# Performance work log

Measured on AMD Instinct MI355X. Metric: run time of the kernel, lower is better.

## Reference

```python
import jax, jax.numpy as jnp
import numpy as np

IOU_THRESHOLD = 0.5  # default in ObjectUtils.nms
N_BOXES = 10000


def setup_inputs() -> dict:
    key = jax.random.key(0)
    k1, k2 = jax.random.split(key)
    boxes = jax.random.uniform(k1, (N_BOXES, 4), dtype=jnp.float32)  # normalized cxcywh
    scores = jax.random.uniform(k2, (N_BOXES,), dtype=jnp.float32)
    return {"boxes_cxcywh": boxes, "scores": scores}


def _cxcywh_to_ltrb(b):
    cx, cy, w, h = b[:, 0], b[:, 1], b[:, 2], b[:, 3]
    return jnp.stack([cx - w / 2, cy - h / 2, cx + w / 2, cy + h / 2], axis=1)


def _pairwise_iou(a, b):
    # a: [N1,4] ltrb, b: [N2,4] ltrb -> [N1,N2] (matches ObjectUtils.compute_iou)
    lt = jnp.maximum(a[:, None, :2], b[None, :, :2])
    rb = jnp.minimum(a[:, None, 2:], b[None, :, 2:])
    wh = jnp.clip(rb - lt, 0.0)
    inter = wh[..., 0] * wh[..., 1]
    area_a = (a[:, 2] - a[:, 0]) * (a[:, 3] - a[:, 1])
    area_b = (b[:, 2] - b[:, 0]) * (b[:, 3] - b[:, 1])
    return inter / (area_a[:, None] + area_b[None, :] - inter)


def reference(boxes_cxcywh, scores):
    ltrb = _cxcywh_to_ltrb(boxes_cxcywh)
    iou = _pairwise_iou(ltrb, ltrb)  # [N,N]

    # ---- greedy NMS, faithful to ObjectUtils.nms (unclamped intersection,
    # retain when iou < threshold) expressed as a jit-friendly suppression loop ----
    n = ltrb.shape[0]
    order = jnp.argsort(-scores)  # highest score first (torch.sort ascending, pop last)
    bs = ltrb[order]
    l, t, r, b = bs[:, 0], bs[:, 1], bs[:, 2], bs[:, 3]
    area = (r - l) * (b - t)
    inter_nms = (jnp.minimum(r[:, None], r[None, :]) - jnp.maximum(l[:, None], l[None, :])) * \
                (jnp.minimum(b[:, None], b[None, :]) - jnp.maximum(t[:, None], t[None, :]))
    iou_nms = inter_nms / (area[:, None] + area[None, :] - inter_nms)
    ar = jnp.arange(n)

    def body(i, keep):
        # box i (in sorted order) suppresses lower-scored boxes only if it is itself kept
        suppress = keep[i] & (iou_nms[i] >= IOU_THRESHOLD) & (ar > i)
        return keep & jnp.logical_not(suppress)

    keep_sorted = jax.lax.fori_loop(0, n, body, jnp.ones((n,), dtype=bool))
    keep = jnp.zeros((n,), dtype=bool).at[order].set(keep_sorted)
    return iou, keep
```

## Files before the change

### kernel.cpp

```cpp
#include <hip/hip_runtime.h>

typedef unsigned long long u64;
typedef float f32x4 __attribute__((ext_vector_type(4)));

#define THR 0.5f

__device__ __forceinline__ u64 rfl64(u64 v) {
  unsigned lo = (unsigned)__builtin_amdgcn_readfirstlane((int)(unsigned)v);
  unsigned hi = (unsigned)__builtin_amdgcn_readfirstlane((int)(unsigned)(v >> 32));
  return ((u64)hi << 32) | lo;
}

__device__ __forceinline__ void conv_box(const float4 b, float& l, float& t,
                                         float& r, float& bo, float& a) {
  #pragma clang fp contract(off)
  float hw = 0.5f * b.z;
  float hh = 0.5f * b.w;
  l = b.x - hw;
  t = b.y - hh;
  r = b.x + hw;
  bo = b.y + hh;
  a = (r - l) * (bo - t);
}

__global__ void k_zero(int* __restrict__ rank, int n) {
  int i = blockIdx.x * blockDim.x + threadIdx.x;
  if (i < n) rank[i] = 0;
}

__global__ void k_rank(const float* __restrict__ scores, int* __restrict__ rank,
                       int n, int jchunk) {
  int i = blockIdx.x * blockDim.x + threadIdx.x;
  if (i >= n) return;
  float si = scores[i];
  int j0 = blockIdx.y * jchunk;
  int j1 = min(j0 + jchunk, n);
  int c = 0;
  for (int j = j0; j < j1; ++j) {
    float sj = scores[j];
    c += ((sj > si) || (sj == si && j < i)) ? 1 : 0;
  }
  if (c) atomicAdd(rank + i, c);
}

__global__ void k_scatter(const float4* __restrict__ boxes, const int* __restrict__ rank,
                          float* __restrict__ sl, float* __restrict__ st,
                          float* __restrict__ sr, float* __restrict__ sb,
                          float* __restrict__ sa, int* __restrict__ sidx, int n) {
  int i = blockIdx.x * blockDim.x + threadIdx.x;
  if (i >= n) return;
  float l, t, r, b, a;
  conv_box(boxes[i], l, t, r, b, a);
  int k = rank[i];
  sl[k] = l; st[k] = t; sr[k] = r; sb[k] = b; sa[k] = a; sidx[k] = i;
}

__device__ __forceinline__ void mask_body(
    const float* __restrict__ sl, const float* __restrict__ st,
    const float* __restrict__ sr, const float* __restrict__ sb,
    const float* __restrict__ sa,
    u64* __restrict__ mask, u64* __restrict__ diag,
    u64* __restrict__ band1, u64* __restrict__ band2,
    int n, int wstride, int bx, int by) {
  #pragma clang fp contract(off)
  int k = bx * 256 + threadIdx.x;
  if (k >= n) return;
  int w = by;
  int jbase = w << 6;
  u64 word = 0;
  if (jbase + 63 > k) {
    float l = sl[k], t = st[k], r = sr[k], b = sb[k], a = sa[k];
    int jend = min(jbase + 64, n);
    for (int j = max(jbase, k + 1); j < jend; ++j) {
      float lmax = fmaxf(l, sl[j]);
      float tmax = fmaxf(t, st[j]);
      float rmin = fminf(r, sr[j]);
      float bmin = fminf(b, sb[j]);
      float wd = rmin - lmax;
      float hd = bmin - tmax;
      float inter = wd * hd;
      float denom = (a + sa[j]) - inter;
      float q = inter / denom;
      if (q >= THR) word |= 1ull << (j - jbase);
    }
  }
  mask[(size_t)k * wstride + w] = word;
  int kg = k >> 6;
  if (kg == w) diag[k] = word;
  if (w == kg + 1) band1[k] = word;
  if (w == kg + 2) band2[k] = word;
}

__global__ void k_mask(const float* __restrict__ sl, const float* __restrict__ st,
                       const float* __restrict__ sr, const float* __restrict__ sb,
                       const float* __restrict__ sa,
                       u64* __restrict__ mask, u64* __restrict__ diag,
                       u64* __restrict__ band1, u64* __restrict__ band2,
                       int n, int wstride) {
  mask_body(sl, st, sr, sb, sa, mask, diag, band1, band2, n, wstride,
            blockIdx.x, blockIdx.y);
}

__device__ __forceinline__ u64 wave_or_u64(u64 v) {
  unsigned lo = (unsigned)v, hi = (unsigned)(v >> 32);
#define DPP_OR(x, ctrl, rmask) \
  x |= (unsigned)__builtin_amdgcn_update_dpp(0, (int)(x), ctrl, rmask, 0xF, true)
  DPP_OR(lo, 0x111, 0xF); DPP_OR(hi, 0x111, 0xF);
  DPP_OR(lo, 0x112, 0xF); DPP_OR(hi, 0x112, 0xF);
  DPP_OR(lo, 0x114, 0xF); DPP_OR(hi, 0x114, 0xF);
  DPP_OR(lo, 0x118, 0xF); DPP_OR(hi, 0x118, 0xF);
  DPP_OR(lo, 0x142, 0xA); DPP_OR(hi, 0x142, 0xA);
  DPP_OR(lo, 0x143, 0xC); DPP_OR(hi, 0x143, 0xC);
#undef DPP_OR
  unsigned flo = (unsigned)__builtin_amdgcn_readlane((int)lo, 63);
  unsigned fhi = (unsigned)__builtin_amdgcn_readlane((int)hi, 63);
  return ((u64)fhi << 32) | flo;
}

__device__ __forceinline__ void scan_body9(
    const u64* __restrict__ mask, const u64* __restrict__ diag,
    const u64* __restrict__ band1, const u64* __restrict__ band2,
    const int* __restrict__ sidx, float* __restrict__ keep,
    int n, int wstride,
    u64* rem, u64* bsh1, u64* bsh2, u64* kwords,
    int (*kept)[64], int* nk_sh) {
  int t = threadIdx.x, wv = t >> 6, lane = t & 63;
  int ng = (n + 63) >> 6;
  rem[t] = 0;
  if (t < 3) nk_sh[t] = 0;
  u64 R1 = 0, R2 = 0;
  u64 A0=0,A1=0,A2=0,A3=0,A4=0,A5=0,A6=0,A7=0;
  u64 B0=0,B1=0,B2=0,B3=0,B4=0,B5=0,B6=0,B7=0;
  u64 C0=0,C1=0,C2=0,C3=0,C4=0,C5=0,C6=0,C7=0;
  if (wv == 0) {
    bsh1[lane] = band1[lane];
    bsh2[lane] = band2[lane];
    A0=diag[0];A1=diag[1];A2=diag[2];A3=diag[3];
    A4=diag[4];A5=diag[5];A6=diag[6];A7=diag[7];
    B0=diag[8];B1=diag[9];B2=diag[10];B3=diag[11];
    B4=diag[12];B5=diag[13];B6=diag[14];B7=diag[15];
  }
  __syncthreads();
  for (int g = 0; g < ng; ++g) {
    int base = g << 6;
    if (wv == 0) {
      int nxt = base + 64 + lane;
      bool hn = (g + 1 < ng);
      u64 b1next = hn ? band1[nxt] : 0;
      u64 b2next = hn ? band2[nxt] : 0;
      u64 b1v = bsh1[lane], b2v = bsh2[lane];
      u64 s = rfl64(rem[g]) | R1;
      int valid = n - base;
      if (valid < 64) s |= (~0ull) << valid;
      u64 kw = 0;
      const u64* __restrict__ dgrp = diag + base;
#define SLOAD(P0,P1,P2,P3,P4,P5,P6,P7, OFF) { \
      P0 = dgrp[(OFF)+0]; P1 = dgrp[(OFF)+1]; P2 = dgrp[(OFF)+2]; P3 = dgrp[(OFF)+3]; \
      P4 = dgrp[(OFF)+4]; P5 = dgrp[(OFF)+5]; P6 = dgrp[(OFF)+6]; P7 = dgrp[(OFF)+7]; }
#define SSTEP(BB, EQ) { u64 sup = (s >> (BB)) & 1ull; \
      kw |= (sup ^ 1ull) << (BB); s |= sup ? 0ull : (EQ); }
#define SCHUNK(B0v, E0,E1,E2,E3,E4,E5,E6,E7) \
      if (((~s >> (B0v)) & 0xFFull) != 0ull) { \
        SSTEP(B0v+0, E0) SSTEP(B0v+1, E1) SSTEP(B0v+2, E2) SSTEP(B0v+3, E3) \
        SSTEP(B0v+4, E4) SSTEP(B0v+5, E5) SSTEP(B0v+6, E6) SSTEP(B0v+7, E7) }
      SLOAD(C0,C1,C2,C3,C4,C5,C6,C7, 16); SCHUNK(0,  A0,A1,A2,A3,A4,A5,A6,A7);
      SLOAD(A0,A1,A2,A3,A4,A5,A6,A7, 24); SCHUNK(8,  B0,B1,B2,B3,B4,B5,B6,B7);
      SLOAD(B0,B1,B2,B3,B4,B5,B6,B7, 32); SCHUNK(16, C0,C1,C2,C3,C4,C5,C6,C7);
      SLOAD(C0,C1,C2,C3,C4,C5,C6,C7, 40); SCHUNK(24, A0,A1,A2,A3,A4,A5,A6,A7);
      SLOAD(A0,A1,A2,A3,A4,A5,A6,A7, 48); SCHUNK(32, B0,B1,B2,B3,B4,B5,B6,B7);
      SLOAD(B0,B1,B2,B3,B4,B5,B6,B7, 56); SCHUNK(40, C0,C1,C2,C3,C4,C5,C6,C7);
                                          SCHUNK(48, A0,A1,A2,A3,A4,A5,A6,A7);
                                          SCHUNK(56, B0,B1,B2,B3,B4,B5,B6,B7);
      SLOAD(A0,A1,A2,A3,A4,A5,A6,A7, 64);
      SLOAD(B0,B1,B2,B3,B4,B5,B6,B7, 72);
#undef SCHUNK
#undef SSTEP
#undef SLOAD
      if (lane == 0) kwords[g] = kw;
      u64 c1 = 0, c2 = 0;
      if (kw) {
        int nk = __popcll(kw);
        if ((kw >> lane) & 1ull) {
          int pos = __popcll(kw & ((1ull << lane) - 1ull));
          kept[g % 3][pos] = lane;
        }
        int npad = (nk + 31) & ~31;
        if (lane >= nk && lane < npad) kept[g % 3][lane] = 0;
        if (lane == 0) nk_sh[g % 3] = nk;
        u64 m = (u64)0 - ((kw >> lane) & 1ull);
        c1 = wave_or_u64(b1v & m);
        c2 = wave_or_u64(b2v & m);
      } else {
        if (lane == 0) nk_sh[g % 3] = 0;
      }
      R1 = R2 | c1;
      R2 = c2;
      bsh1[lane] = b1next;
      bsh2[lane] = b2next;
    } else {
      int w = t - 64;
      int gp = g - 2;
      if (gp >= 0 && w > g && w < ng) {
        int nkp = nk_sh[gp % 3];
        if (nkp) {
          const int* kp = kept[gp % 3];
          int basep = gp << 6;
          u64 acc = 0;
          for (int i = 0; i < nkp; i += 32) {
#define LD1(q) u64 v##q = mask[(size_t)(basep + kp[i + q]) * wstride + w];
            LD1(0)  LD1(1)  LD1(2)  LD1(3)  LD1(4)  LD1(5)  LD1(6)  LD1(7)
            LD1(8)  LD1(9)  LD1(10) LD1(11) LD1(12) LD1(13) LD1(14) LD1(15)
            LD1(16) LD1(17) LD1(18) LD1(19) LD1(20) LD1(21) LD1(22) LD1(23)
            LD1(24) LD1(25) LD1(26) LD1(27) LD1(28) LD1(29) LD1(30) LD1(31)
#undef LD1
#define ACC(q) if (i + q < nkp) acc |= v##q;
            ACC(0)  ACC(1)  ACC(2)  ACC(3)  ACC(4)  ACC(5)  ACC(6)  ACC(7)
            ACC(8)  ACC(9)  ACC(10) ACC(11) ACC(12) ACC(13) ACC(14) ACC(15)
            ACC(16) ACC(17) ACC(18) ACC(19) ACC(20) ACC(21) ACC(22) ACC(23)
            ACC(24) ACC(25) ACC(26) ACC(27) ACC(28) ACC(29) ACC(30) ACC(31)
#undef ACC
          }
          rem[w] |= acc;
        }
      }
    }
    __syncthreads();
  }
  for (int k = t; k < n; k += 256) {
    u64 kwv = kwords[k >> 6];
    keep[sidx[k]] = ((kwv >> (k & 63)) & 1ull) ? 1.0f : 0.0f;
  }
}

__global__ __launch_bounds__(256, 1) void k_scan2(const u64* __restrict__ mask,
                                                  const u64* __restrict__ diag,
                                                  const u64* __restrict__ band1,
                                                  const u64* __restrict__ band2,
                                                  const int* __restrict__ sidx,
                                                  float* __restrict__ keep,
                                                  int n, int wstride) {
  __shared__ u64 rem[256];
  __shared__ u64 bsh1[64];
  __shared__ u64 bsh2[64];
  __shared__ u64 kwords[160];
  __shared__ int kept[3][64];
  __shared__ int nk_sh[3];
  scan_body9(mask, diag, band1, band2, sidx, keep, n, wstride,
             rem, bsh1, bsh2, kwords, kept, nk_sh);
}

__device__ __forceinline__ float iou_one(float li, float ti, float ri, float bi, float ai,
                                         float lj, float tj, float rj, float bj, float aj) {
  float lmax = fmaxf(li, lj);
  float tmax = fmaxf(ti, tj);
  float rmin = fminf(ri, rj);
  float bmin = fminf(bi, bj);
  float w = fmaxf(rmin - lmax, 0.0f);
  float h = fmaxf(bmin - tmax, 0.0f);
  float inter = w * h;
  float denom = (ai + aj) - inter;
  return inter * __builtin_amdgcn_rcpf(denom);
}

__device__ __forceinline__ void iou_body(const float4* __restrict__ boxes,
                                         float* __restrict__ out,
                                         int n, int rpb, int bx, int by) {
  int nj4 = (n + 3) >> 2;
  int j4 = bx * 256 + threadIdx.x;
  if (j4 >= nj4) return;
  int j = j4 << 2;
  int jc1 = min(j + 1, n - 1), jc2 = min(j + 2, n - 1), jc3 = min(j + 3, n - 1);
  float l0,t0,r0,b0,a0, l1,t1,r1,b1,a1, l2,t2,r2,b2,a2, l3,t3,r3,b3,a3;
  conv_box(boxes[j],   l0,t0,r0,b0,a0);
  conv_box(boxes[jc1], l1,t1,r1,b1,a1);
  conv_box(boxes[jc2], l2,t2,r2,b2,a2);
  conv_box(boxes[jc3], l3,t3,r3,b3,a3);
  bool full = (j + 3) < n;
  for (int rr = 0; rr < rpb; ++rr) {
    int i = by * rpb + rr;
    if (i >= n) return;
    float li,ti,ri,bi,ai;
    conv_box(boxes[i], li,ti,ri,bi,ai);
    float4 o;
    o.x = iou_one(li,ti,ri,bi,ai, l0,t0,r0,b0,a0);
    o.y = iou_one(li,ti,ri,bi,ai, l1,t1,r1,b1,a1);
    o.z = iou_one(li,ti,ri,bi,ai, l2,t2,r2,b2,a2);
    o.w = iou_one(li,ti,ri,bi,ai, l3,t3,r3,b3,a3);
    size_t row = (size_t)i * n;
    if (full) {
      f32x4 ov = { o.x, o.y, o.z, o.w };
      __builtin_nontemporal_store(ov, reinterpret_cast<f32x4*>(out + row + j));
    } else {
      out[row + j] = o.x;
      if (j + 1 < n) out[row + j + 1] = o.y;
      if (j + 2 < n) out[row + j + 2] = o.z;
    }
  }
}

__global__ void k_iou(const float4* __restrict__ boxes, float* __restrict__ out,
                      int n, int rpb) {
  iou_body(boxes, out, n, rpb, blockIdx.x, blockIdx.y);
}

__global__ __launch_bounds__(256) void k_maskiou(
    const float* __restrict__ sl, const float* __restrict__ st,
    const float* __restrict__ sr, const float* __restrict__ sb,
    const float* __restrict__ sa,
    u64* __restrict__ mask, u64* __restrict__ diag,
    u64* __restrict__ band1, u64* __restrict__ band2,
    int wstride, const float4* __restrict__ boxes, float* __restrict__ out,
    int n, int rpb, int nbx, int nmask, int gx) {
  int id = blockIdx.x;
  if (id < nmask) {
    mask_body(sl, st, sr, sb, sa, mask, diag, band1, band2, n, wstride,
              id % nbx, id / nbx);
  } else {
    int iid = id - nmask;
    iou_body(boxes, out, n, rpb, iid % gx, iid / gx);
  }
}

extern "C" void kernel_launch(void* const* d_in, const int* in_sizes, int n_in,
                              void* d_out, int out_size, void* d_ws, size_t ws_size,
                              hipStream_t stream) {
  const float* boxes = (const float*)d_in[0];
  const float* scores = (const float*)d_in[1];
  int n = in_sizes[1];
  float* out = (float*)d_out;
  size_t NN = (size_t)n * (size_t)n;
  float* keep = out + NN;

  int words = (n + 63) >> 6;
  int wstride = (words + 3) & ~3;
  size_t need = (size_t)n * wstride * 8
              + ((size_t)words * 64 + 64) * 8
              + (size_t)words * 64 * 8 * 2
              + 256
              + (size_t)n * 4 * 7;
  bool use_ws = (ws_size >= need);

  char* base = use_ws ? (char*)d_ws : (char*)d_out;
  size_t off = 0;
  u64* mask  = (u64*)(base + off); off += (size_t)n * wstride * 8;
  u64* diag  = (u64*)(base + off); off += ((size_t)words * 64 + 64) * 8;
  u64* band1 = (u64*)(base + off); off += (size_t)words * 64 * 8;
  u64* band2 = (u64*)(base + off); off += (size_t)words * 64 * 8;
  off = (off + 255) & ~(size_t)255;
  float* sl  = (float*)(base + off); off += (size_t)n * 4;
  float* st_ = (float*)(base + off); off += (size_t)n * 4;
  float* sr  = (float*)(base + off); off += (size_t)n * 4;
  float* sb  = (float*)(base + off); off += (size_t)n * 4;
  float* sa  = (float*)(base + off); off += (size_t)n * 4;
  int* sidx  = (int*)(base + off); off += (size_t)n * 4;
  int* rank  = (int*)(base + off); off += (size_t)n * 4;

  int nb = (n + 255) / 256;
  k_zero<<<nb, 256, 0, stream>>>(rank, n);

  int jblocks = 40;
  int jchunk = (n + jblocks - 1) / jblocks;
  k_rank<<<dim3(nb, jblocks), 256, 0, stream>>>(scores, rank, n, jchunk);

  k_scatter<<<nb, 256, 0, stream>>>((const float4*)boxes, rank, sl, st_, sr, sb, sa, sidx, n);

  int rpb = 10;
  int nj4 = (n + 3) >> 2;
  int gx = (nj4 + 255) / 256;
  int gy = (n + rpb - 1) / rpb;

  if (use_ws) {
    int nmask = nb * words;
    int total = nmask + gx * gy;
    k_maskiou<<<total, 256, 0, stream>>>(sl, st_, sr, sb, sa, mask, diag, band1,
                                         band2, wstride, (const float4*)boxes,
                                         out, n, rpb, nb, nmask, gx);
    k_scan2<<<1, 256, 0, stream>>>(mask, diag, band1, band2, sidx, keep, n, wstride);
  } else {
    k_mask<<<dim3(nb, words), 256, 0, stream>>>(sl, st_, sr, sb, sa, mask, diag,
                                                band1, band2, n, wstride);
    k_scan2<<<1, 256, 0, stream>>>(mask, diag, band1, band2, sidx, keep, n, wstride);
    k_iou<<<dim3(gx, gy), 256, 0, stream>>>((const float4*)boxes, out, n, rpb);
  }
}
```

Before: 455.9 us.

## Replace 4-wave NMS scan with single-wave register-resident scan

```diff
diff --git a/kernel.cpp b/kernel.cpp
--- a/kernel.cpp
+++ b/kernel.cpp
@@ -5,9 +5,9 @@
 
 #define THR 0.5f
 
-__device__ __forceinline__ u64 rfl64(u64 v) {
-  unsigned lo = (unsigned)__builtin_amdgcn_readfirstlane((int)(unsigned)v);
-  unsigned hi = (unsigned)__builtin_amdgcn_readfirstlane((int)(unsigned)(v >> 32));
+__device__ __forceinline__ u64 rdl64c(u64 v, int l) {
+  unsigned lo = (unsigned)__builtin_amdgcn_readlane((int)(unsigned)v, l);
+  unsigned hi = (unsigned)__builtin_amdgcn_readlane((int)(unsigned)(v >> 32), l);
   return ((u64)hi << 32) | lo;
 }
 
@@ -117,136 +117,177 @@
   return ((u64)fhi << 32) | flo;
 }
 
-__device__ __forceinline__ void scan_body9(
+__device__ __forceinline__ void fold8_now(const u64* __restrict__ mask, int base,
+    u64 bits, int cnt, int wstride, int lane, int w2c,
+    u64& r0, u64& r1, u64& r2) {
+  u64 t = bits;
+  int k0 = __ffsll((long long)t) - 1; t &= t - 1;
+  int k1 = __ffsll((long long)t) - 1; t &= t - 1;
+  int k2 = __ffsll((long long)t) - 1; t &= t - 1;
+  int k3 = __ffsll((long long)t) - 1; t &= t - 1;
+  int k4 = __ffsll((long long)t) - 1; t &= t - 1;
+  int k5 = __ffsll((long long)t) - 1; t &= t - 1;
+  int k6 = __ffsll((long long)t) - 1; t &= t - 1;
+  int k7 = __ffsll((long long)t) - 1;
+  k0 = max(k0, 0); k1 = max(k1, 0); k2 = max(k2, 0); k3 = max(k3, 0);
+  k4 = max(k4, 0); k5 = max(k5, 0); k6 = max(k6, 0); k7 = max(k7, 0);
+  const u64* p0 = mask + (size_t)(base + k0) * wstride;
+  const u64* p1 = mask + (size_t)(base + k1) * wstride;
+  const u64* p2 = mask + (size_t)(base + k2) * wstride;
+  const u64* p3 = mask + (size_t)(base + k3) * wstride;
+  const u64* p4 = mask + (size_t)(base + k4) * wstride;
+  const u64* p5 = mask + (size_t)(base + k5) * wstride;
+  const u64* p6 = mask + (size_t)(base + k6) * wstride;
+  const u64* p7 = mask + (size_t)(base + k7) * wstride;
+  u64 a0=p0[lane], a1=p0[lane+64], a2=p0[w2c];
+  u64 b0=p1[lane], b1=p1[lane+64], b2=p1[w2c];
+  u64 c0=p2[lane], c1=p2[lane+64], c2=p2[w2c];
+  u64 d0=p3[lane], d1=p3[lane+64], d2=p3[w2c];
+  u64 e0=p4[lane], e1=p4[lane+64], e2=p4[w2c];
+  u64 f0=p5[lane], f1=p5[lane+64], f2=p5[w2c];
+  u64 g0=p6[lane], g1=p6[lane+64], g2=p6[w2c];
+  u64 h0=p7[lane], h1=p7[lane+64], h2=p7[w2c];
+  if (cnt > 0) { r0|=a0; r1|=a1; r2|=a2; }
+  if (cnt > 1) { r0|=b0; r1|=b1; r2|=b2; }
+  if (cnt > 2) { r0|=c0; r1|=c1; r2|=c2; }
+  if (cnt > 3) { r0|=d0; r1|=d1; r2|=d2; }
+  if (cnt > 4) { r0|=e0; r1|=e1; r2|=e2; }
+  if (cnt > 5) { r0|=f0; r1|=f1; r2|=f2; }
+  if (cnt > 6) { r0|=g0; r1|=g1; r2|=g2; }
+  if (cnt > 7) { r0|=h0; r1|=h1; r2|=h2; }
+}
+
+__global__ __launch_bounds__(64, 1) void k_scan3(
     const u64* __restrict__ mask, const u64* __restrict__ diag,
     const u64* __restrict__ band1, const u64* __restrict__ band2,
     const int* __restrict__ sidx, float* __restrict__ keep,
-    int n, int wstride,
-    u64* rem, u64* bsh1, u64* bsh2, u64* kwords,
-    int (*kept)[64], int* nk_sh) {
-  int t = threadIdx.x, wv = t >> 6, lane = t & 63;
+    int n, int wstride) {
+  int lane = threadIdx.x;
   int ng = (n + 63) >> 6;
-  rem[t] = 0;
-  if (t < 3) nk_sh[t] = 0;
+  int words = ng;
+  int w2c = min(lane + 128, words - 1);
+  u64 r0 = 0, r1 = 0, r2 = 0;
   u64 R1 = 0, R2 = 0;
-  u64 A0=0,A1=0,A2=0,A3=0,A4=0,A5=0,A6=0,A7=0;
-  u64 B0=0,B1=0,B2=0,B3=0,B4=0,B5=0,B6=0,B7=0;
-  u64 C0=0,C1=0,C2=0,C3=0,C4=0,C5=0,C6=0,C7=0;
-  if (wv == 0) {
-    bsh1[lane] = band1[lane];
-    bsh2[lane] = band2[lane];
-    A0=diag[0];A1=diag[1];A2=diag[2];A3=diag[3];
-    A4=diag[4];A5=diag[5];A6=diag[6];A7=diag[7];
-    B0=diag[8];B1=diag[9];B2=diag[10];B3=diag[11];
-    B4=diag[12];B5=diag[13];B6=diag[14];B7=diag[15];
-  }
-  __syncthreads();
+  u64 d_cur = diag[lane],  d_nx = diag[64 + lane];
+  u64 b1_cur = band1[lane], b1_nx = band1[64 + lane];
+  u64 b2_cur = band2[lane], b2_nx = band2[64 + lane];
+  int sx_cur = (lane < n) ? sidx[lane] : 0;
+  int sx_nx  = (64 + lane < n) ? sidx[64 + lane] : 0;
+  u64 fA00=0,fA01=0,fA02=0,fA10=0,fA11=0,fA12=0,fA20=0,fA21=0,fA22=0,
+      fA30=0,fA31=0,fA32=0,fA40=0,fA41=0,fA42=0,fA50=0,fA51=0,fA52=0,
+      fA60=0,fA61=0,fA62=0,fA70=0,fA71=0,fA72=0;
+  u64 fB00=0,fB01=0,fB02=0,fB10=0,fB11=0,fB12=0,fB20=0,fB21=0,fB22=0,
+      fB30=0,fB31=0,fB32=0,fB40=0,fB41=0,fB42=0,fB50=0,fB51=0,fB52=0,
+      fB60=0,fB61=0,fB62=0,fB70=0,fB71=0,fB72=0;
+  int nkA = 0, nkB = 0;
+
   for (int g = 0; g < ng; ++g) {
     int base = g << 6;
-    if (wv == 0) {
-      int nxt = base + 64 + lane;
-      bool hn = (g + 1 < ng);
-      u64 b1next = hn ? band1[nxt] : 0;
-      u64 b2next = hn ? band2[nxt] : 0;
-      u64 b1v = bsh1[lane], b2v = bsh2[lane];
-      u64 s = rfl64(rem[g]) | R1;
-      int valid = n - base;
-      if (valid < 64) s |= (~0ull) << valid;
-      u64 kw = 0;
-      const u64* __restrict__ dgrp = diag + base;
-#define SLOAD(P0,P1,P2,P3,P4,P5,P6,P7, OFF) { \
-      P0 = dgrp[(OFF)+0]; P1 = dgrp[(OFF)+1]; P2 = dgrp[(OFF)+2]; P3 = dgrp[(OFF)+3]; \
-      P4 = dgrp[(OFF)+4]; P5 = dgrp[(OFF)+5]; P6 = dgrp[(OFF)+6]; P7 = dgrp[(OFF)+7]; }
+    if ((g & 1) == 0) {
+      if (nkA > 0) { r0|=fA00; r1|=fA01; r2|=fA02; }
+      if (nkA > 1) { r0|=fA10; r1|=fA11; r2|=fA12; }
+      if (nkA > 2) { r0|=fA20; r1|=fA21; r2|=fA22; }
+      if (nkA > 3) { r0|=fA30; r1|=fA31; r2|=fA32; }
+      if (nkA > 4) { r0|=fA40; r1|=fA41; r2|=fA42; }
+      if (nkA > 5) { r0|=fA50; r1|=fA51; r2|=fA52; }
+      if (nkA > 6) { r0|=fA60; r1|=fA61; r2|=fA62; }
+      if (nkA > 7) { r0|=fA70; r1|=fA71; r2|=fA72; }
+      nkA = 0;
+    } else {
+      if (nkB > 0) { r0|=fB00; r1|=fB01; r2|=fB02; }
+      if (nkB > 1) { r0|=fB10; r1|=fB11; r2|=fB12; }
+      if (nkB > 2) { r0|=fB20; r1|=fB21; r2|=fB22; }
+      if (nkB > 3) { r0|=fB30; r1|=fB31; r2|=fB32; }
+      if (nkB > 4) { r0|=fB40; r1|=fB41; r2|=fB42; }
+      if (nkB > 5) { r0|=fB50; r1|=fB51; r2|=fB52; }
+      if (nkB > 6) { r0|=fB60; r1|=fB61; r2|=fB62; }
+      if (nkB > 7) { r0|=fB70; r1|=fB71; r2|=fB72; }
+      nkB = 0;
+    }
+    u64 rr = (g < 64) ? r0 : (g < 128) ? r1 : r2;
+    u64 s = rdl64c(rr, g & 63) | R1;
+    int valid = n - base;
+    if (valid < 64) s |= (~0ull) << valid;
+    u64 kw = 0;
 #define SSTEP(BB, EQ) { u64 sup = (s >> (BB)) & 1ull; \
-      kw |= (sup ^ 1ull) << (BB); s |= sup ? 0ull : (EQ); }
-#define SCHUNK(B0v, E0,E1,E2,E3,E4,E5,E6,E7) \
-      if (((~s >> (B0v)) & 0xFFull) != 0ull) { \
-        SSTEP(B0v+0, E0) SSTEP(B0v+1, E1) SSTEP(B0v+2, E2) SSTEP(B0v+3, E3) \
-        SSTEP(B0v+4, E4) SSTEP(B0v+5, E5) SSTEP(B0v+6, E6) SSTEP(B0v+7, E7) }
-      SLOAD(C0,C1,C2,C3,C4,C5,C6,C7, 16); SCHUNK(0,  A0,A1,A2,A3,A4,A5,A6,A7);
-      SLOAD(A0,A1,A2,A3,A4,A5,A6,A7, 24); SCHUNK(8,  B0,B1,B2,B3,B4,B5,B6,B7);
-      SLOAD(B0,B1,B2,B3,B4,B5,B6,B7, 32); SCHUNK(16, C0,C1,C2,C3,C4,C5,C6,C7);
-      SLOAD(C0,C1,C2,C3,C4,C5,C6,C7, 40); SCHUNK(24, A0,A1,A2,A3,A4,A5,A6,A7);
-      SLOAD(A0,A1,A2,A3,A4,A5,A6,A7, 48); SCHUNK(32, B0,B1,B2,B3,B4,B5,B6,B7);
-      SLOAD(B0,B1,B2,B3,B4,B5,B6,B7, 56); SCHUNK(40, C0,C1,C2,C3,C4,C5,C6,C7);
-                                          SCHUNK(48, A0,A1,A2,A3,A4,A5,A6,A7);
-                                          SCHUNK(56, B0,B1,B2,B3,B4,B5,B6,B7);
-      SLOAD(A0,A1,A2,A3,A4,A5,A6,A7, 64);
-      SLOAD(B0,B1,B2,B3,B4,B5,B6,B7, 72);
+    kw |= (sup ^ 1ull) << (BB); s |= sup ? 0ull : (EQ); }
+#define SCHUNK(B0v) \
+    if (((~s >> (B0v)) & 0xFFull) != 0ull) { \
+      u64 E0 = rdl64c(d_cur, (B0v)+0); u64 E1 = rdl64c(d_cur, (B0v)+1); \
+      u64 E2 = rdl64c(d_cur, (B0v)+2); u64 E3 = rdl64c(d_cur, (B0v)+3); \
+      u64 E4 = rdl64c(d_cur, (B0v)+4); u64 E5 = rdl64c(d_cur, (B0v)+5); \
+      u64 E6 = rdl64c(d_cur, (B0v)+6); u64 E7 = rdl64c(d_cur, (B0v)+7); \
+      SSTEP((B0v)+0, E0) SSTEP((B0v)+1, E1) SSTEP((B0v)+2, E2) SSTEP((B0v)+3, E3) \
+      SSTEP((B0v)+4, E4) SSTEP((B0v)+5, E5) SSTEP((B0v)+6, E6) SSTEP((B0v)+7, E7) }
+    SCHUNK(0) SCHUNK(8) SCHUNK(16) SCHUNK(24)
+    SCHUNK(32) SCHUNK(40) SCHUNK(48) SCHUNK(56)
 #undef SCHUNK
 #undef SSTEP
-#undef SLOAD
-      if (lane == 0) kwords[g] = kw;
-      u64 c1 = 0, c2 = 0;
-      if (kw) {
-        int nk = __popcll(kw);
-        if ((kw >> lane) & 1ull) {
-          int pos = __popcll(kw & ((1ull << lane) - 1ull));
-          kept[g % 3][pos] = lane;
-        }
-        int npad = (nk + 31) & ~31;
-        if (lane >= nk && lane < npad) kept[g % 3][lane] = 0;
-        if (lane == 0) nk_sh[g % 3] = nk;
-        u64 m = (u64)0 - ((kw >> lane) & 1ull);
-        c1 = wave_or_u64(b1v & m);
-        c2 = wave_or_u64(b2v & m);
+    if (base + lane < n) keep[sx_cur] = ((kw >> lane) & 1ull) ? 1.0f : 0.0f;
+    u64 m = (u64)0 - ((kw >> lane) & 1ull);
+    u64 c1 = wave_or_u64(b1_cur & m);
+    u64 c2 = wave_or_u64(b2_cur & m);
+    R1 = R2 | c1;
+    R2 = c2;
+    int nk = __popcll(kw);
+    if (nk > 0) {
+      u64 t = kw;
+      int kk0 = __ffsll((long long)t) - 1; t &= t - 1;
+      int kk1 = __ffsll((long long)t) - 1; t &= t - 1;
+      int kk2 = __ffsll((long long)t) - 1; t &= t - 1;
+      int kk3 = __ffsll((long long)t) - 1; t &= t - 1;
+      int kk4 = __ffsll((long long)t) - 1; t &= t - 1;
+      int kk5 = __ffsll((long long)t) - 1; t &= t - 1;
+      int kk6 = __ffsll((long long)t) - 1; t &= t - 1;
+      int kk7 = __ffsll((long long)t) - 1; t &= t - 1;
+      kk0 = max(kk0,0); kk1 = max(kk1,0); kk2 = max(kk2,0); kk3 = max(kk3,0);
+      kk4 = max(kk4,0); kk5 = max(kk5,0); kk6 = max(kk6,0); kk7 = max(kk7,0);
+      const u64* p0 = mask + (size_t)(base + kk0) * wstride;
+      const u64* p1 = mask + (size_t)(base + kk1) * wstride;
+      const u64* p2 = mask + (size_t)(base + kk2) * wstride;
+      const u64* p3 = mask + (size_t)(base + kk3) * wstride;
+      const u64* p4 = mask + (size_t)(base + kk4) * wstride;
+      const u64* p5 = mask + (size_t)(base + kk5) * wstride;
+      const u64* p6 = mask + (size_t)(base + kk6) * wstride;
+      const u64* p7 = mask + (size_t)(base + kk7) * wstride;
+      if ((g & 1) == 0) {
+        fA00=p0[lane]; fA01=p0[lane+64]; fA02=p0[w2c];
+        fA10=p1[lane]; fA11=p1[lane+64]; fA12=p1[w2c];
+        fA20=p2[lane]; fA21=p2[lane+64]; fA22=p2[w2c];
+        fA30=p3[lane]; fA31=p3[lane+64]; fA32=p3[w2c];
+        fA40=p4[lane]; fA41=p4[lane+64]; fA42=p4[w2c];
+        fA50=p5[lane]; fA51=p5[lane+64]; fA52=p5[w2c];
+        fA60=p6[lane]; fA61=p6[lane+64]; fA62=p6[w2c];
+        fA70=p7[lane]; fA71=p7[lane+64]; fA72=p7[w2c];
+        nkA = min(nk, 8);
       } else {
-        if (lane == 0) nk_sh[g % 3] = 0;
+        fB00=p0[lane]; fB01=p0[lane+64]; fB02=p0[w2c];
+        fB10=p1[lane]; fB11=p1[lane+64]; fB12=p1[w2c];
+        fB20=p2[lane]; fB21=p2[lane+64]; fB22=p2[w2c];
+        fB30=p3[lane]; fB31=p3[lane+64]; fB32=p3[w2c];
+        fB40=p4[lane]; fB41=p4[lane+64]; fB42=p4[w2c];
+        fB50=p5[lane]; fB51=p5[lane+64]; fB52=p5[w2c];
+        fB60=p6[lane]; fB61=p6[lane+64]; fB62=p6[w2c];
+        fB70=p7[lane]; fB71=p7[lane+64]; fB72=p7[w2c];
+        nkB = min(nk, 8);
       }
-      R1 = R2 | c1;
-      R2 = c2;
-      bsh1[lane] = b1next;
-      bsh2[lane] = b2next;
+      int remn = nk - 8;
+      while (remn > 0) {
+        fold8_now(mask, base, t, remn, wstride, lane, w2c, r0, r1, r2);
+        #pragma unroll
+        for (int j = 0; j < 8; ++j) t &= t - 1;
+        remn -= 8;
+      }
     } else {
-      int w = t - 64;
-      int gp = g - 2;
-      if (gp >= 0 && w > g && w < ng) {
-        int nkp = nk_sh[gp % 3];
-        if (nkp) {
-          const int* kp = kept[gp % 3];
-          int basep = gp << 6;
-          u64 acc = 0;
-          for (int i = 0; i < nkp; i += 32) {
-#define LD1(q) u64 v##q = mask[(size_t)(basep + kp[i + q]) * wstride + w];
-            LD1(0)  LD1(1)  LD1(2)  LD1(3)  LD1(4)  LD1(5)  LD1(6)  LD1(7)
-            LD1(8)  LD1(9)  LD1(10) LD1(11) LD1(12) LD1(13) LD1(14) LD1(15)
-            LD1(16) LD1(17) LD1(18) LD1(19) LD1(20) LD1(21) LD1(22) LD1(23)
-            LD1(24) LD1(25) LD1(26) LD1(27) LD1(28) LD1(29) LD1(30) LD1(31)
-#undef LD1
-#define ACC(q) if (i + q < nkp) acc |= v##q;
-            ACC(0)  ACC(1)  ACC(2)  ACC(3)  ACC(4)  ACC(5)  ACC(6)  ACC(7)
-            ACC(8)  ACC(9)  ACC(10) ACC(11) ACC(12) ACC(13) ACC(14) ACC(15)
-            ACC(16) ACC(17) ACC(18) ACC(19) ACC(20) ACC(21) ACC(22) ACC(23)
-            ACC(24) ACC(25) ACC(26) ACC(27) ACC(28) ACC(29) ACC(30) ACC(31)
-#undef ACC
-          }
-          rem[w] |= acc;
-        }
-      }
+      if ((g & 1) == 0) nkA = 0; else nkB = 0;
     }
-    __syncthreads();
-  }
-  for (int k = t; k < n; k += 256) {
-    u64 kwv = kwords[k >> 6];
-    keep[sidx[k]] = ((kwv >> (k & 63)) & 1ull) ? 1.0f : 0.0f;
-  }
-}
-
-__global__ __launch_bounds__(256, 1) void k_scan2(const u64* __restrict__ mask,
-                                                  const u64* __restrict__ diag,
-                                                  const u64* __restrict__ band1,
-                                                  const u64* __restrict__ band2,
-                                                  const int* __restrict__ sidx,
-                                                  float* __restrict__ keep,
-                                                  int n, int wstride) {
-  __shared__ u64 rem[256];
-  __shared__ u64 bsh1[64];
-  __shared__ u64 bsh2[64];
-  __shared__ u64 kwords[160];
-  __shared__ int kept[3][64];
-  __shared__ int nk_sh[3];
-  scan_body9(mask, diag, band1, band2, sidx, keep, n, wstride,
-             rem, bsh1, bsh2, kwords, kept, nk_sh);
+    d_cur = d_nx;   d_nx  = diag[base + 128 + lane];
+    b1_cur = b1_nx; b1_nx = band1[base + 128 + lane];
+    b2_cur = b2_nx; b2_nx = band2[base + 128 + lane];
+    sx_cur = sx_nx;
+    int nxt2 = base + 128 + lane;
+    sx_nx = (nxt2 < n) ? sidx[nxt2] : 0;
+  }
 }
 
 __device__ __forceinline__ float iou_one(float li, float ti, float ri, float bi, float ai,
@@ -333,9 +374,9 @@
 
   int words = (n + 63) >> 6;
   int wstride = (words + 3) & ~3;
+  size_t dbsz = (size_t)words * 64 + 128;
   size_t need = (size_t)n * wstride * 8
-              + ((size_t)words * 64 + 64) * 8
-              + (size_t)words * 64 * 8 * 2
+              + dbsz * 8 * 3
               + 256
               + (size_t)n * 4 * 7;
   bool use_ws = (ws_size >= need);
@@ -343,9 +384,9 @@
   char* base = use_ws ? (char*)d_ws : (char*)d_out;
   size_t off = 0;
   u64* mask  = (u64*)(base + off); off += (size_t)n * wstride * 8;
-  u64* diag  = (u64*)(base + off); off += ((size_t)words * 64 + 64) * 8;
-  u64* band1 = (u64*)(base + off); off += (size_t)words * 64 * 8;
-  u64* band2 = (u64*)(base + off); off += (size_t)words * 64 * 8;
+  u64* diag  = (u64*)(base + off); off += dbsz * 8;
+  u64* band1 = (u64*)(base + off); off += dbsz * 8;
+  u64* band2 = (u64*)(base + off); off += dbsz * 8;
   off = (off + 255) & ~(size_t)255;
   float* sl  = (float*)(base + off); off += (size_t)n * 4;
   float* st_ = (float*)(base + off); off += (size_t)n * 4;
@@ -375,11 +416,11 @@
     k_maskiou<<<total, 256, 0, stream>>>(sl, st_, sr, sb, sa, mask, diag, band1,
                                          band2, wstride, (const float4*)boxes,
                                          out, n, rpb, nb, nmask, gx);
-    k_scan2<<<1, 256, 0, stream>>>(mask, diag, band1, band2, sidx, keep, n, wstride);
+    k_scan3<<<1, 64, 0, stream>>>(mask, diag, band1, band2, sidx, keep, n, wstride);
   } else {
     k_mask<<<dim3(nb, words), 256, 0, stream>>>(sl, st_, sr, sb, sa, mask, diag,
                                                 band1, band2, n, wstride);
-    k_scan2<<<1, 256, 0, stream>>>(mask, diag, band1, band2, sidx, keep, n, wstride);
+    k_scan3<<<1, 64, 0, stream>>>(mask, diag, band1, band2, sidx, keep, n, wstride);
     k_iou<<<dim3(gx, gy), 256, 0, stream>>>((const float4*)boxes, out, n, rpb);
   }
 }
```

Result: slower. 546.0 us (+19.8%).
